# Optimization experiments

Hardware: AMD Instinct MI355X
Metric: run time of the kernel (lower is better)

The kernel has to match this reference:

```python
import jax, jax.numpy as jnp
import numpy as np

OUTPUT_SIZE = 256  # D: softmax / reduction dim (init arg output_size)


def setup_inputs() -> dict:
    key = jax.random.key(0)
    k1, k2 = jax.random.split(key)
    S = jax.random.normal(k1, (8192, OUTPUT_SIZE), dtype=jnp.float32)
    V = jax.random.normal(k2, (8192, OUTPUT_SIZE), dtype=jnp.float32)
    return {"S": S, "V": V}


def reference(S, V):
    # Original torch module: S, V viewed to (-1, D); for each pair (i, j)
    # it runs an online-softmax (flash-attention style) recurrence over D,
    # computing O[i, j] = sum_k softmax(S[i])_k * V[j, k].
    # Vectorized: O = softmax(S, -1) @ V.T  -> shape [N, M]
    D = S.shape[-1]
    S2 = S.reshape(-1, D)  # [N, D]
    V2 = V.reshape(-1, D)  # [M, D]
    P = jax.nn.softmax(S2, axis=-1)  # stable online-softmax equivalent
    return jnp.einsum('nd,md->nm', P, V2)
```

## Files before the change

kernel.cpp:

```cpp
#include <hip/hip_runtime.h>

typedef __attribute__((ext_vector_type(8))) short bf16x8;
typedef __attribute__((ext_vector_type(4))) float f32x4;

#define D_DIM 256
#define NROW  8192

__device__ __forceinline__ unsigned short f2bf(float x) {
  unsigned int u = __float_as_uint(x);
  u += 0x7fffu + ((u >> 16) & 1u);
  return (unsigned short)(u >> 16);
}

__device__ __forceinline__ void gload_lds16(const void* g, void* l) {
  __builtin_amdgcn_global_load_lds((__attribute__((address_space(1))) void*)g,
                                   (__attribute__((address_space(3))) void*)l,
                                   16, 0, 0);
}

__global__ __launch_bounds__(256) void softmax_rows(const float* __restrict__ S,
                                                    unsigned short* __restrict__ P) {
  const int row  = blockIdx.x * 4 + (threadIdx.x >> 6);
  const int lane = threadIdx.x & 63;
  float4 v = ((const float4*)(S + row * D_DIM))[lane];
  float m = fmaxf(fmaxf(v.x, v.y), fmaxf(v.z, v.w));
#pragma unroll
  for (int off = 32; off > 0; off >>= 1) m = fmaxf(m, __shfl_xor(m, off));
  float e0 = __expf(v.x - m), e1 = __expf(v.y - m);
  float e2 = __expf(v.z - m), e3 = __expf(v.w - m);
  float s = e0 + e1 + e2 + e3;
#pragma unroll
  for (int off = 32; off > 0; off >>= 1) s += __shfl_xor(s, off);
  const float inv = 1.0f / s;
  ushort4 o;
  o.x = f2bf(e0 * inv); o.y = f2bf(e1 * inv);
  o.z = f2bf(e2 * inv); o.w = f2bf(e3 * inv);
  ((ushort4*)(P + row * D_DIM))[lane] = o;
}

__global__ __launch_bounds__(256) void cast_v(const float* __restrict__ V,
                                              unsigned short* __restrict__ Vb) {
  const int i = blockIdx.x * 256 + threadIdx.x;
  float4 v = ((const float4*)V)[i];
  ushort4 o;
  o.x = f2bf(v.x); o.y = f2bf(v.y); o.z = f2bf(v.z); o.w = f2bf(v.w);
  ((ushort4*)Vb)[i] = o;
}


__device__ __forceinline__ void stage_tile(const unsigned short* ga,
                                           const unsigned short* gb,
                                           unsigned short* la, int ko) {
  gload_lds16(ga + ko,              la);
  gload_lds16(ga + 32 * D_DIM + ko, la + 2048);
  gload_lds16(ga + 64 * D_DIM + ko, la + 4096);
  gload_lds16(ga + 96 * D_DIM + ko, la + 6144);
  gload_lds16(gb + ko,              la + 8192);
  gload_lds16(gb + 32 * D_DIM + ko, la + 8192 + 2048);
  gload_lds16(gb + 64 * D_DIM + ko, la + 8192 + 4096);
  gload_lds16(gb + 96 * D_DIM + ko, la + 8192 + 6144);
}

__device__ __forceinline__ void compute_tile(const unsigned short* __restrict__ A_,
                                             const unsigned short* __restrict__ B_,
                                             int arow, int brow, int k16,
                                             f32x4 acc[4][4]) {
#pragma unroll
  for (int j = 0; j < 2; ++j) {
    bf16x8 af[4], bfr[4];
#pragma unroll
    for (int mi = 0; mi < 4; ++mi) {
      const int r = arow + mi * 16;
      af[mi] = *(const bf16x8*)&A_[r * 64 + ((j * 32 + k16) ^ ((r & 7) * 8))];
    }
#pragma unroll
    for (int ni = 0; ni < 4; ++ni) {
      const int r = brow + ni * 16;
      bfr[ni] = *(const bf16x8*)&B_[r * 64 + ((j * 32 + k16) ^ ((r & 7) * 8))];
    }
#pragma unroll
    for (int mi = 0; mi < 4; ++mi)
#pragma unroll
      for (int ni = 0; ni < 4; ++ni)
        acc[mi][ni] = __builtin_amdgcn_mfma_f32_16x16x32_bf16(af[mi], bfr[ni],
                                                              acc[mi][ni], 0, 0, 0);
  }
}

__global__ __launch_bounds__(256) void gemm_bt(const unsigned short* __restrict__ P,
                                               const unsigned short* __restrict__ Vb,
                                               float* __restrict__ O) {
  __shared__ unsigned short smem[32768];

  const int t    = threadIdx.x;
  const int lane = t & 63;
  const int wave = t >> 6;
  const int wm   = (wave & 1) * 64;
  const int wn   = (wave >> 1) * 64;

  const int id  = blockIdx.x;
  const int xcd = id & 7;
  const int q   = id >> 3;
  const int bm  = xcd * 8 + (q & 7);
  const int bn  = q >> 3;

  f32x4 acc[4][4] = {};

  const int srow = t >> 3;
  const int xg   = ((t & 7) * 8) ^ ((srow & 7) * 8);
  const unsigned short* ga = P  + (size_t)(bm * 128 + srow) * D_DIM + xg;
  const unsigned short* gb = Vb + (size_t)(bn * 128 + srow) * D_DIM + xg;
  unsigned short* l0 = smem + t * 8;

  const int arow = wm + (lane & 15);
  const int brow = wn + (lane & 15);
  const int k16  = (lane >> 4) * 8;

  stage_tile(ga, gb, l0, 0);
  asm volatile("s_waitcnt vmcnt(0)" ::: "memory");
  __builtin_amdgcn_s_barrier();
  __builtin_amdgcn_sched_barrier(0);

  stage_tile(ga, gb, l0 + 16384, 64);
  compute_tile(smem, smem + 8192, arow, brow, k16, acc);
  asm volatile("s_waitcnt vmcnt(0)" ::: "memory");
  __builtin_amdgcn_s_barrier();
  __builtin_amdgcn_sched_barrier(0);

  stage_tile(ga, gb, l0, 128);
  compute_tile(smem + 16384, smem + 24576, arow, brow, k16, acc);
  asm volatile("s_waitcnt vmcnt(0)" ::: "memory");
  __builtin_amdgcn_s_barrier();
  __builtin_amdgcn_sched_barrier(0);

  stage_tile(ga, gb, l0 + 16384, 192);
  compute_tile(smem, smem + 8192, arow, brow, k16, acc);
  asm volatile("s_waitcnt vmcnt(0)" ::: "memory");
  __builtin_amdgcn_s_barrier();
  __builtin_amdgcn_sched_barrier(0);

  compute_tile(smem + 16384, smem + 24576, arow, brow, k16, acc);

  __syncthreads();

  float* smf = (float*)smem;
  float* ep  = smf + wave * 2176;
  const int qrow = (lane >> 4) * 4;
  const int qcol = lane & 15;
  const size_t orow0 = (size_t)(bm * 128 + wm);
  const int    ocol0 = bn * 128 + wn + (lane & 15) * 4;

#pragma unroll
  for (int p = 0; p < 2; ++p) {
#pragma unroll
    for (int mi2 = 0; mi2 < 2; ++mi2) {
      const int mi = p * 2 + mi2;
      const int r0 = mi2 * 16 + qrow;
#pragma unroll
      for (int ni = 0; ni < 4; ++ni)
#pragma unroll
        for (int r = 0; r < 4; ++r)
          ep[(r0 + r) * 68 + ni * 16 + qcol] = acc[mi][ni][r];
    }
#pragma unroll
    for (int qq = 0; qq < 8; ++qq) {
      const int rl = qq * 4 + (lane >> 4);
      float4 vv = *(const float4*)&ep[rl * 68 + (lane & 15) * 4];
      *(float4*)&O[(orow0 + p * 32 + rl) * NROW + ocol0] = vv;
    }
    if (p == 0) __syncthreads();
  }
}

extern "C" void kernel_launch(void* const* d_in, const int* in_sizes, int n_in,
                              void* d_out, int out_size, void* d_ws, size_t ws_size,
                              hipStream_t stream) {
  const float* S = (const float*)d_in[0];
  const float* V = (const float*)d_in[1];
  float* O = (float*)d_out;

  unsigned short* P  = (unsigned short*)d_ws;
  unsigned short* Vb = P + (size_t)NROW * D_DIM;

  softmax_rows<<<NROW / 4, 256, 0, stream>>>(S, P);
  cast_v<<<(NROW * D_DIM / 4) / 256, 256, 0, stream>>>(V, Vb);
  gemm_bt<<<NROW / 128 * (NROW / 128), 256, 0, stream>>>(P, Vb, O);
}
```

Before: 289.2 us.

## Shrink GEMM K-tile to 32 with 8-stage double buffer and nontemporal output stores

Cuts the GEMM's LDS footprint from 64KB to 32KB by staging K in 32-wide chunks across an 8-iteration double-buffered loop. Adds launch_bounds occupancy 4 and a matching XOR swizzle for the narrower rows. The epilogue now goes through a smaller per-wave staging buffer, one 16-row slice at a time with no mid-epilogue barrier, and writes O with nontemporal stores. The goal is more resident blocks per CU and less cache pollution from the large fp32 output. The cost is twice as many barriers per K sweep and less work per barrier interval.

New measurement: 289.4 us. About the same (+0.1%).

```diff
diff --git a/kernel.cpp b/kernel.cpp
--- a/kernel.cpp
+++ b/kernel.cpp
@@ -47,50 +47,10 @@
   ((ushort4*)Vb)[i] = o;
 }
 
-
-__device__ __forceinline__ void stage_tile(const unsigned short* ga,
-                                           const unsigned short* gb,
-                                           unsigned short* la, int ko) {
-  gload_lds16(ga + ko,              la);
-  gload_lds16(ga + 32 * D_DIM + ko, la + 2048);
-  gload_lds16(ga + 64 * D_DIM + ko, la + 4096);
-  gload_lds16(ga + 96 * D_DIM + ko, la + 6144);
-  gload_lds16(gb + ko,              la + 8192);
-  gload_lds16(gb + 32 * D_DIM + ko, la + 8192 + 2048);
-  gload_lds16(gb + 64 * D_DIM + ko, la + 8192 + 4096);
-  gload_lds16(gb + 96 * D_DIM + ko, la + 8192 + 6144);
-}
-
-__device__ __forceinline__ void compute_tile(const unsigned short* __restrict__ A_,
-                                             const unsigned short* __restrict__ B_,
-                                             int arow, int brow, int k16,
-                                             f32x4 acc[4][4]) {
-#pragma unroll
-  for (int j = 0; j < 2; ++j) {
-    bf16x8 af[4], bfr[4];
-#pragma unroll
-    for (int mi = 0; mi < 4; ++mi) {
-      const int r = arow + mi * 16;
-      af[mi] = *(const bf16x8*)&A_[r * 64 + ((j * 32 + k16) ^ ((r & 7) * 8))];
-    }
-#pragma unroll
-    for (int ni = 0; ni < 4; ++ni) {
-      const int r = brow + ni * 16;
-      bfr[ni] = *(const bf16x8*)&B_[r * 64 + ((j * 32 + k16) ^ ((r & 7) * 8))];
-    }
-#pragma unroll
-    for (int mi = 0; mi < 4; ++mi)
-#pragma unroll
-      for (int ni = 0; ni < 4; ++ni)
-        acc[mi][ni] = __builtin_amdgcn_mfma_f32_16x16x32_bf16(af[mi], bfr[ni],
-                                                              acc[mi][ni], 0, 0, 0);
-  }
-}
-
-__global__ __launch_bounds__(256) void gemm_bt(const unsigned short* __restrict__ P,
-                                               const unsigned short* __restrict__ Vb,
-                                               float* __restrict__ O) {
-  __shared__ unsigned short smem[32768];
+__global__ __launch_bounds__(256, 4) void gemm_bt(const unsigned short* __restrict__ P,
+                                                  const unsigned short* __restrict__ Vb,
+                                                  float* __restrict__ O) {
+  __shared__ unsigned short smem[16384];
 
   const int t    = threadIdx.x;
   const int lane = t & 63;
@@ -106,69 +66,84 @@
 
   f32x4 acc[4][4] = {};
 
-  const int srow = t >> 3;
-  const int xg   = ((t & 7) * 8) ^ ((srow & 7) * 8);
+  const int srow = t >> 2;
+  const int xg   = (((t & 3) ^ ((srow >> 1) & 3)) * 8);
   const unsigned short* ga = P  + (size_t)(bm * 128 + srow) * D_DIM + xg;
   const unsigned short* gb = Vb + (size_t)(bn * 128 + srow) * D_DIM + xg;
   unsigned short* l0 = smem + t * 8;
 
   const int arow = wm + (lane & 15);
   const int brow = wn + (lane & 15);
-  const int k16  = (lane >> 4) * 8;
+  const int kch  = lane >> 4;
 
-  stage_tile(ga, gb, l0, 0);
-  asm volatile("s_waitcnt vmcnt(0)" ::: "memory");
-  __builtin_amdgcn_s_barrier();
-  __builtin_amdgcn_sched_barrier(0);
+  {
+    gload_lds16(ga, l0);
+    gload_lds16(ga + 64 * D_DIM, l0 + 2048);
+    gload_lds16(gb, l0 + 4096);
+    gload_lds16(gb + 64 * D_DIM, l0 + 6144);
+    asm volatile("s_waitcnt vmcnt(0)" ::: "memory");
+    __builtin_amdgcn_s_barrier();
+    __builtin_amdgcn_sched_barrier(0);
+  }
 
-  stage_tile(ga, gb, l0 + 16384, 64);
-  compute_tile(smem, smem + 8192, arow, brow, k16, acc);
-  asm volatile("s_waitcnt vmcnt(0)" ::: "memory");
-  __builtin_amdgcn_s_barrier();
-  __builtin_amdgcn_sched_barrier(0);
-
-  stage_tile(ga, gb, l0, 128);
-  compute_tile(smem + 16384, smem + 24576, arow, brow, k16, acc);
-  asm volatile("s_waitcnt vmcnt(0)" ::: "memory");
-  __builtin_amdgcn_s_barrier();
-  __builtin_amdgcn_sched_barrier(0);
-
-  stage_tile(ga, gb, l0 + 16384, 192);
-  compute_tile(smem, smem + 8192, arow, brow, k16, acc);
-  asm volatile("s_waitcnt vmcnt(0)" ::: "memory");
-  __builtin_amdgcn_s_barrier();
-  __builtin_amdgcn_sched_barrier(0);
-
-  compute_tile(smem + 16384, smem + 24576, arow, brow, k16, acc);
+#pragma unroll
+  for (int tk = 0; tk < 8; ++tk) {
+    const unsigned short* cur = smem + (tk & 1) * 8192;
+    unsigned short*       nxt = l0 + ((tk & 1) ^ 1) * 8192;
+    if (tk < 7) {
+      const int ko = (tk + 1) * 32;
+      gload_lds16(ga + ko,               nxt);
+      gload_lds16(ga + 64 * D_DIM + ko,  nxt + 2048);
+      gload_lds16(gb + ko,               nxt + 4096);
+      gload_lds16(gb + 64 * D_DIM + ko,  nxt + 6144);
+    }
+    bf16x8 af[4], bfr[4];
+#pragma unroll
+    for (int mi = 0; mi < 4; ++mi) {
+      const int r = arow + mi * 16;
+      af[mi] = *(const bf16x8*)&cur[r * 32 + ((kch ^ ((r >> 1) & 3)) * 8)];
+    }
+#pragma unroll
+    for (int ni = 0; ni < 4; ++ni) {
+      const int r = brow + ni * 16;
+      bfr[ni] = *(const bf16x8*)&cur[4096 + r * 32 + ((kch ^ ((r >> 1) & 3)) * 8)];
+    }
+#pragma unroll
+    for (int mi = 0; mi < 4; ++mi)
+#pragma unroll
+      for (int ni = 0; ni < 4; ++ni)
+        acc[mi][ni] = __builtin_amdgcn_mfma_f32_16x16x32_bf16(af[mi], bfr[ni],
+                                                              acc[mi][ni], 0, 0, 0);
+    if (tk < 7) {
+      asm volatile("s_waitcnt vmcnt(0)" ::: "memory");
+      __builtin_amdgcn_s_barrier();
+      __builtin_amdgcn_sched_barrier(0);
+    }
+  }
 
   __syncthreads();
 
   float* smf = (float*)smem;
-  float* ep  = smf + wave * 2176;
+  float* ep  = smf + wave * 1088;
   const int qrow = (lane >> 4) * 4;
   const int qcol = lane & 15;
   const size_t orow0 = (size_t)(bm * 128 + wm);
   const int    ocol0 = bn * 128 + wn + (lane & 15) * 4;
 
 #pragma unroll
-  for (int p = 0; p < 2; ++p) {
+  for (int mi = 0; mi < 4; ++mi) {
 #pragma unroll
-    for (int mi2 = 0; mi2 < 2; ++mi2) {
-      const int mi = p * 2 + mi2;
-      const int r0 = mi2 * 16 + qrow;
+    for (int ni = 0; ni < 4; ++ni)
 #pragma unroll
-      for (int ni = 0; ni < 4; ++ni)
+      for (int r = 0; r < 4; ++r)
+        ep[(qrow + r) * 68 + ni * 16 + qcol] = acc[mi][ni][r];
 #pragma unroll
-        for (int r = 0; r < 4; ++r)
-          ep[(r0 + r) * 68 + ni * 16 + qcol] = acc[mi][ni][r];
+    for (int qq = 0; qq < 4; ++qq) {
+      const int rl = qq * 4 + (lane >> 4);
+      f32x4 vv = *(const f32x4*)&ep[rl * 68 + (lane & 15) * 4];
+      __builtin_nontemporal_store(vv,
+          (f32x4*)&O[(orow0 + mi * 16 + rl) * NROW + ocol0]);
     }
-#pragma unroll
-    for (int qq = 0; qq < 8; ++qq) {
-      const int rl = qq * 4 + (lane >> 4);
-      float4 vv = *(const float4*)&ep[rl * 68 + (lane & 15) * 4];
-      *(float4*)&O[(orow0 + p * 32 + rl) * NROW + ocol0] = vv;
-    }
-    if (p == 0) __syncthreads();
   }
 }
 
```
